# Performance work log

Hardware: AMD Instinct MI355X
Metric: run time of the kernel (lower is better)

## Reference

```python
import jax, jax.numpy as jnp
import numpy as np

B, M, K = 32, 64, 36
DS, DX, DQ, H = 512, 128, 512, 256


def setup_inputs() -> dict:
    key = jax.random.key(0)
    ks = jax.random.split(key, 11)
    sc = lambda fan_in: 1.0 / np.sqrt(fan_in)
    return {
        "s2": jax.random.normal(ks[0], (B, M, DS), jnp.float32),
        "x0": jax.random.normal(ks[1], (B, K, DX), jnp.float32),
        "q": jax.random.normal(ks[2], (B, DQ), jnp.float32),
        # score MLP: Linear(DS+DX+DQ -> H), ReLU, Linear(H -> 1)
        "score_w1": jax.random.normal(ks[3], (DS + DX + DQ, H), jnp.float32) * sc(DS + DX + DQ),
        "score_b1": jax.random.normal(ks[4], (H,), jnp.float32) * 0.01,
        "score_w2": jax.random.normal(ks[5], (H, 1), jnp.float32) * sc(H),
        "score_b2": jax.random.normal(ks[6], (1,), jnp.float32) * 0.01,
        # h MLP: Linear(DS -> H), ReLU, Linear(H -> DX)
        "h_w1": jax.random.normal(ks[7], (DS, H), jnp.float32) * sc(DS),
        "h_b1": jax.random.normal(ks[8], (H,), jnp.float32) * 0.01,
        "h_w2": jax.random.normal(ks[9], (H, DX), jnp.float32) * sc(H),
        "h_b2": jax.random.normal(ks[10], (DX,), jnp.float32) * 0.01,
    }


def reference(s2, x0, q, score_w1, score_b1, score_w2, score_b2, h_w1, h_b1, h_w2, h_b2):
    ds = s2.shape[-1]
    dx = x0.shape[-1]
    # First score Linear over concat [s_exp, x_exp, q_exp] decomposes into
    # block matmuls (same math as Linear on the concat, no 4D concat tensor).
    w_s = score_w1[:ds]            # (DS, H)
    w_x = score_w1[ds:ds + dx]     # (DX, H)
    w_q = score_w1[ds + dx:]       # (DQ, H)
    pre_s = jnp.einsum('bmd,dh->bmh', s2, w_s)   # (b, m, H)
    pre_x = jnp.einsum('bkd,dh->bkh', x0, w_x)   # (b, k, H)
    pre_q = q @ w_q                              # (b, H)
    hidden = jax.nn.relu(pre_s[:, :, None, :] + pre_x[:, None, :, :]
                         + pre_q[:, None, None, :] + score_b1)  # (b, m, k, H)
    logits = jnp.einsum('bmkh,h->bmk', hidden, score_w2[:, 0]) + score_b2[0]
    att = jax.nn.softmax(logits, axis=1)         # softmax over m
    h_s = jax.nn.relu(s2 @ h_w1 + h_b1) @ h_w2 + h_b2  # (b, m, DX)
    agg = jnp.einsum('bmk,bmf->bkf', att, h_s)   # (b, k, DX)
    return jnp.concatenate([x0, agg], axis=-1)   # (b, k, 2*DX)
```

## Files before the change

kernel.cpp:

```cpp
#include <hip/hip_runtime.h>

#define B_  32
#define M_  64
#define K_  36
#define DS_ 512
#define DX_ 128
#define DQ_ 512
#define H_  256

#define TMA  16
#define DCH  128
#define KB   9

__global__ __launch_bounds__(256) void kernA(
    const float* __restrict__ s2,
    const float* __restrict__ score_w1,
    const float* __restrict__ h_w1,
    const float* __restrict__ q,
    const float* __restrict__ score_b1,
    const float* __restrict__ x0,
    float* __restrict__ pre_s,
    float* __restrict__ ph1,
    float* __restrict__ cvec)
{
    const int t   = threadIdx.x;
    const int bid = blockIdx.x;

    if (bid >= 1024) {
        const int cb = bid - 1024;
        const int b  = cb >> 2;
        const int kq = cb & 3;
        const float* qp = q + (size_t)b * DQ_;
        const float* wq = score_w1 + (size_t)(DS_ + DX_) * H_ + t;
        float a0 = score_b1[t], a1 = 0.f, a2 = 0.f, a3 = 0.f;
        for (int d = 0; d < DQ_; d += 4) {
            const float4 q4 = *(const float4*)(qp + d);
            a0 = fmaf(q4.x, wq[(size_t)(d + 0) * H_], a0);
            a1 = fmaf(q4.y, wq[(size_t)(d + 1) * H_], a1);
            a2 = fmaf(q4.z, wq[(size_t)(d + 2) * H_], a2);
            a3 = fmaf(q4.w, wq[(size_t)(d + 3) * H_], a3);
        }
        const float qacc = (a0 + a1) + (a2 + a3);

        float acc[KB];
        #pragma unroll
        for (int kk = 0; kk < KB; ++kk) acc[kk] = qacc;

        const float* xsrc = x0 + ((size_t)b * K_ + kq * KB) * DX_;
        const float* wx   = score_w1 + (size_t)DS_ * H_ + t;
        for (int d = 0; d < DX_; d += 4) {
            const float w0 = wx[(size_t)(d + 0) * H_];
            const float w1 = wx[(size_t)(d + 1) * H_];
            const float w2v = wx[(size_t)(d + 2) * H_];
            const float w3 = wx[(size_t)(d + 3) * H_];
            #pragma unroll
            for (int kk = 0; kk < KB; ++kk) {
                const float4 x4 = *(const float4*)(xsrc + (size_t)kk * DX_ + d);
                acc[kk] = fmaf(x4.x, w0, acc[kk]);
                acc[kk] = fmaf(x4.y, w1, acc[kk]);
                acc[kk] = fmaf(x4.z, w2v, acc[kk]);
                acc[kk] = fmaf(x4.w, w3, acc[kk]);
            }
        }
        #pragma unroll
        for (int kk = 0; kk < KB; ++kk)
            cvec[((size_t)b * K_ + kq * KB + kk) * H_ + t] = acc[kk];
        return;
    }

    const int tile = bid >> 3;
    const int mat  = bid & 1;
    const int dq   = (bid >> 1) & 3;

    const float* w  = (mat ? h_w1 : score_w1) + (size_t)(dq * DCH) * H_ + t;
    const float* sp = s2 + (size_t)tile * TMA * DS_ + dq * DCH;

    float acc[TMA];
    #pragma unroll
    for (int i = 0; i < TMA; ++i) acc[i] = 0.f;

    for (int d = 0; d < DCH; d += 4) {
        const float w0 = w[(size_t)(d + 0) * H_];
        const float w1 = w[(size_t)(d + 1) * H_];
        const float w2v = w[(size_t)(d + 2) * H_];
        const float w3 = w[(size_t)(d + 3) * H_];
        #pragma unroll
        for (int i = 0; i < TMA; ++i) {
            const float4 s4 = *(const float4*)(sp + (size_t)i * DS_ + d);
            acc[i] = fmaf(s4.x, w0, acc[i]);
            acc[i] = fmaf(s4.y, w1, acc[i]);
            acc[i] = fmaf(s4.z, w2v, acc[i]);
            acc[i] = fmaf(s4.w, w3, acc[i]);
        }
    }

    float* dst = (mat ? ph1 : pre_s) + (size_t)tile * TMA * H_ + t;
    #pragma unroll
    for (int i = 0; i < TMA; ++i)
        atomicAdd(dst + (size_t)i * H_, acc[i]);
}

__global__ __launch_bounds__(256) void kernH(
    const float* __restrict__ ph1,
    const float* __restrict__ h_b1,
    const float* __restrict__ h_w2,
    float* __restrict__ h_s)
{
    __shared__ float sh[4][DCH];
    const int t    = threadIdx.x;
    const int tile = blockIdx.x >> 1;
    const int hh   = blockIdx.x & 1;
    const int r0   = tile * 4;

    if (t < 128) {
        const int row = t >> 5, j4 = (t & 31) * 4;
        const float4 p = *(const float4*)(ph1 + (size_t)(r0 + row) * H_ + hh * DCH + j4);
        const float4 b = *(const float4*)(h_b1 + hh * DCH + j4);
        float4 r;
        r.x = fmaxf(p.x + b.x, 0.f);
        r.y = fmaxf(p.y + b.y, 0.f);
        r.z = fmaxf(p.z + b.z, 0.f);
        r.w = fmaxf(p.w + b.w, 0.f);
        *(float4*)&sh[row][j4] = r;
    }
    __syncthreads();

    const int f  = t & 127;
    const int rp = t >> 7;
    const float* wp = h_w2 + (size_t)(hh * DCH) * DX_ + f;
    float acc0 = 0.f, acc1 = 0.f;
    #pragma unroll 4
    for (int h = 0; h < DCH; ++h) {
        const float wv = wp[(size_t)h * DX_];
        acc0 = fmaf(sh[rp * 2 + 0][h], wv, acc0);
        acc1 = fmaf(sh[rp * 2 + 1][h], wv, acc1);
    }
    atomicAdd(h_s + (size_t)(r0 + rp * 2 + 0) * DX_ + f, acc0);
    atomicAdd(h_s + (size_t)(r0 + rp * 2 + 1) * DX_ + f, acc1);
}

__global__ __launch_bounds__(256) void kernC(
    const float* __restrict__ pre_s,
    const float* __restrict__ h_s,
    const float* __restrict__ cvec,
    const float* __restrict__ score_w2,
    const float* __restrict__ h_b2,
    const float* __restrict__ x0,
    float* __restrict__ out)
{
    __shared__ float  red[M_][65];
    __shared__ float  att[M_];
    __shared__ float4 part[8][32];

    const int t    = threadIdx.x;
    const int bk   = blockIdx.x;
    const int b    = bk / K_;
    const int wave = t >> 6, lane = t & 63;

    const float4 cf = *(const float4*)(cvec + (size_t)bk * H_ + 4 * lane);
    const float4 wf = *(const float4*)(score_w2 + 4 * lane);

    const float* ps = pre_s + (size_t)b * M_ * H_;
    #pragma unroll 4
    for (int mi = 0; mi < M_ / 4; ++mi) {
        const int m = wave * (M_ / 4) + mi;
        const float4 p = *(const float4*)(ps + (size_t)m * H_ + 4 * lane);
        red[m][lane] = fmaxf(p.x + cf.x, 0.f) * wf.x
                     + fmaxf(p.y + cf.y, 0.f) * wf.y
                     + fmaxf(p.z + cf.z, 0.f) * wf.z
                     + fmaxf(p.w + cf.w, 0.f) * wf.w;
    }
    __syncthreads();

    if (wave == 0) {
        float a0 = 0.f, a1 = 0.f, a2 = 0.f, a3 = 0.f;
        #pragma unroll 4
        for (int l = 0; l < 64; l += 4) {
            a0 += red[lane][l + 0];
            a1 += red[lane][l + 1];
            a2 += red[lane][l + 2];
            a3 += red[lane][l + 3];
        }
        const float L = (a0 + a1) + (a2 + a3);
        float mx = L;
        #pragma unroll
        for (int off = 32; off > 0; off >>= 1)
            mx = fmaxf(mx, __shfl_xor(mx, off, 64));
        const float e = expf(L - mx);
        float s = e;
        #pragma unroll
        for (int off = 32; off > 0; off >>= 1)
            s += __shfl_xor(s, off, 64);
        att[lane] = e / s;
    }
    __syncthreads();

    {
        const int g = t >> 5, l32 = t & 31;
        const float* hp = h_s + ((size_t)b * M_ + g * 8) * DX_ + 4 * l32;
        float4 acc = make_float4(0.f, 0.f, 0.f, 0.f);
        #pragma unroll
        for (int j = 0; j < 8; ++j) {
            const float a = att[g * 8 + j];
            const float4 hv = *(const float4*)(hp + (size_t)j * DX_);
            acc.x = fmaf(a, hv.x, acc.x);
            acc.y = fmaf(a, hv.y, acc.y);
            acc.z = fmaf(a, hv.z, acc.z);
            acc.w = fmaf(a, hv.w, acc.w);
        }
        part[g][l32] = acc;
    }
    __syncthreads();

    const float4* x04 = (const float4*)(x0 + (size_t)bk * DX_);
    float4* o4 = (float4*)(out + (size_t)bk * 2 * DX_);
    if (t < 32) {
        float4 s = part[0][t];
        #pragma unroll
        for (int j = 1; j < 8; ++j) {
            const float4 p = part[j][t];
            s.x += p.x; s.y += p.y; s.z += p.z; s.w += p.w;
        }
        const float4 b2 = *(const float4*)(h_b2 + 4 * t);
        s.x += b2.x; s.y += b2.y; s.z += b2.z; s.w += b2.w;
        o4[32 + t] = s;
    } else if (t < 64) {
        o4[t - 32] = x04[t - 32];
    }
}

extern "C" void kernel_launch(void* const* d_in, const int* in_sizes, int n_in,
                              void* d_out, int out_size, void* d_ws, size_t ws_size,
                              hipStream_t stream) {
    (void)in_sizes; (void)n_in; (void)out_size; (void)ws_size;
    const float* s2       = (const float*)d_in[0];
    const float* x0       = (const float*)d_in[1];
    const float* q        = (const float*)d_in[2];
    const float* score_w1 = (const float*)d_in[3];
    const float* score_b1 = (const float*)d_in[4];
    const float* score_w2 = (const float*)d_in[5];
    const float* h_w1     = (const float*)d_in[7];
    const float* h_b1     = (const float*)d_in[8];
    const float* h_w2     = (const float*)d_in[9];
    const float* h_b2     = (const float*)d_in[10];
    float* out = (float*)d_out;

    float* ws    = (float*)d_ws;
    float* pre_s = ws;
    float* ph1   = pre_s + (size_t)B_ * M_ * H_;
    float* h_s   = ph1   + (size_t)B_ * M_ * H_;
    float* cvec  = h_s   + (size_t)B_ * M_ * DX_;

    hipMemsetAsync(d_ws, 0,
                   (size_t)B_ * M_ * (H_ + H_ + DX_) * sizeof(float), stream);

    kernA<<<1152, 256, 0, stream>>>(s2, score_w1, h_w1, q, score_b1, x0,
                                    pre_s, ph1, cvec);
    kernH<<<1024, 256, 0, stream>>>(ph1, h_b1, h_w2, h_s);
    kernC<<<B_ * K_, 256, 0, stream>>>(pre_s, h_s, cvec, score_w2, h_b2,
                                       x0, out);
}
```

Baseline: 139.5 us.

## Fold second h-MLP layer after attention, drop kernH, retile s2 GEMM

```diff
diff --git a/kernel.cpp b/kernel.cpp
--- a/kernel.cpp
+++ b/kernel.cpp
@@ -11,6 +11,12 @@
 #define TMA  16
 #define DCH  128
 #define KB   9
+
+#define FMA4(acc, sv, wv)              \
+    acc.x = fmaf(sv, wv.x, acc.x);     \
+    acc.y = fmaf(sv, wv.y, acc.y);     \
+    acc.z = fmaf(sv, wv.z, acc.z);     \
+    acc.w = fmaf(sv, wv.w, acc.w);
 
 __global__ __launch_bounds__(256) void kernA(
     const float* __restrict__ s2,
@@ -26,8 +32,8 @@
     const int t   = threadIdx.x;
     const int bid = blockIdx.x;
 
-    if (bid >= 1024) {
-        const int cb = bid - 1024;
+    if (bid < 128) {
+        const int cb = bid;
         const int b  = cb >> 2;
         const int kq = cb & 3;
         const float* qp = q + (size_t)b * DQ_;
@@ -68,89 +74,68 @@
         return;
     }
 
-    const int tile = bid >> 3;
-    const int mat  = bid & 1;
-    const int dq   = (bid >> 1) & 3;
-
-    const float* w  = (mat ? h_w1 : score_w1) + (size_t)(dq * DCH) * H_ + t;
-    const float* sp = s2 + (size_t)tile * TMA * DS_ + dq * DCH;
-
-    float acc[TMA];
+    const int g    = bid - 128;
+    const int tile = g & 127;
+    const int mc   = g >> 7;
+    const int mat  = mc & 1;
+    const int dq   = mc >> 1;
+    const int lane = t & 63;
+    const int wid  = __builtin_amdgcn_readfirstlane(t >> 6);
+
+    const float4* wq = (const float4*)((mat ? h_w1 : score_w1)
+                                       + (size_t)(dq * DCH) * H_ + 4 * lane);
+    const float* srow = s2 + (size_t)(tile * TMA + wid * 4) * DS_ + dq * DCH;
+
+    float4 acc0 = {0,0,0,0}, acc1 = {0,0,0,0}, acc2 = {0,0,0,0}, acc3 = {0,0,0,0};
+    float4 c0 = wq[0], c1 = wq[64], c2 = wq[128], c3 = wq[192];
+
+    for (int d4 = 0; d4 < DCH; d4 += 4) {
+        const int dn = (d4 + 4 < DCH) ? d4 + 4 : d4;
+        const float4 n0 = wq[(size_t)(dn + 0) * 64];
+        const float4 n1 = wq[(size_t)(dn + 1) * 64];
+        const float4 n2 = wq[(size_t)(dn + 2) * 64];
+        const float4 n3 = wq[(size_t)(dn + 3) * 64];
+
+        const float4 s0 = *(const float4*)(srow + 0 * DS_ + d4);
+        const float4 s1 = *(const float4*)(srow + 1 * DS_ + d4);
+        const float4 s2v = *(const float4*)(srow + 2 * DS_ + d4);
+        const float4 s3 = *(const float4*)(srow + 3 * DS_ + d4);
+
+        FMA4(acc0, s0.x, c0)  FMA4(acc0, s0.y, c1)  FMA4(acc0, s0.z, c2)  FMA4(acc0, s0.w, c3)
+        FMA4(acc1, s1.x, c0)  FMA4(acc1, s1.y, c1)  FMA4(acc1, s1.z, c2)  FMA4(acc1, s1.w, c3)
+        FMA4(acc2, s2v.x, c0) FMA4(acc2, s2v.y, c1) FMA4(acc2, s2v.z, c2) FMA4(acc2, s2v.w, c3)
+        FMA4(acc3, s3.x, c0)  FMA4(acc3, s3.y, c1)  FMA4(acc3, s3.z, c2)  FMA4(acc3, s3.w, c3)
+
+        c0 = n0; c1 = n1; c2 = n2; c3 = n3;
+    }
+
+    float* dst = (mat ? ph1 : pre_s)
+               + (size_t)(tile * TMA + wid * 4) * H_ + 4 * lane;
     #pragma unroll
-    for (int i = 0; i < TMA; ++i) acc[i] = 0.f;
-
-    for (int d = 0; d < DCH; d += 4) {
-        const float w0 = w[(size_t)(d + 0) * H_];
-        const float w1 = w[(size_t)(d + 1) * H_];
-        const float w2v = w[(size_t)(d + 2) * H_];
-        const float w3 = w[(size_t)(d + 3) * H_];
-        #pragma unroll
-        for (int i = 0; i < TMA; ++i) {
-            const float4 s4 = *(const float4*)(sp + (size_t)i * DS_ + d);
-            acc[i] = fmaf(s4.x, w0, acc[i]);
-            acc[i] = fmaf(s4.y, w1, acc[i]);
-            acc[i] = fmaf(s4.z, w2v, acc[i]);
-            acc[i] = fmaf(s4.w, w3, acc[i]);
-        }
-    }
-
-    float* dst = (mat ? ph1 : pre_s) + (size_t)tile * TMA * H_ + t;
-    #pragma unroll
-    for (int i = 0; i < TMA; ++i)
-        atomicAdd(dst + (size_t)i * H_, acc[i]);
+    for (int r = 0; r < 4; ++r) {
+        const float4 a = (r == 0) ? acc0 : (r == 1) ? acc1 : (r == 2) ? acc2 : acc3;
+        atomicAdd(dst + (size_t)r * H_ + 0, a.x);
+        atomicAdd(dst + (size_t)r * H_ + 1, a.y);
+        atomicAdd(dst + (size_t)r * H_ + 2, a.z);
+        atomicAdd(dst + (size_t)r * H_ + 3, a.w);
+    }
 }
 
-__global__ __launch_bounds__(256) void kernH(
+__global__ __launch_bounds__(256) void kernC(
+    const float* __restrict__ pre_s,
     const float* __restrict__ ph1,
+    const float* __restrict__ cvec,
+    const float* __restrict__ score_w2,
     const float* __restrict__ h_b1,
     const float* __restrict__ h_w2,
-    float* __restrict__ h_s)
-{
-    __shared__ float sh[4][DCH];
-    const int t    = threadIdx.x;
-    const int tile = blockIdx.x >> 1;
-    const int hh   = blockIdx.x & 1;
-    const int r0   = tile * 4;
-
-    if (t < 128) {
-        const int row = t >> 5, j4 = (t & 31) * 4;
-        const float4 p = *(const float4*)(ph1 + (size_t)(r0 + row) * H_ + hh * DCH + j4);
-        const float4 b = *(const float4*)(h_b1 + hh * DCH + j4);
-        float4 r;
-        r.x = fmaxf(p.x + b.x, 0.f);
-        r.y = fmaxf(p.y + b.y, 0.f);
-        r.z = fmaxf(p.z + b.z, 0.f);
-        r.w = fmaxf(p.w + b.w, 0.f);
-        *(float4*)&sh[row][j4] = r;
-    }
-    __syncthreads();
-
-    const int f  = t & 127;
-    const int rp = t >> 7;
-    const float* wp = h_w2 + (size_t)(hh * DCH) * DX_ + f;
-    float acc0 = 0.f, acc1 = 0.f;
-    #pragma unroll 4
-    for (int h = 0; h < DCH; ++h) {
-        const float wv = wp[(size_t)h * DX_];
-        acc0 = fmaf(sh[rp * 2 + 0][h], wv, acc0);
-        acc1 = fmaf(sh[rp * 2 + 1][h], wv, acc1);
-    }
-    atomicAdd(h_s + (size_t)(r0 + rp * 2 + 0) * DX_ + f, acc0);
-    atomicAdd(h_s + (size_t)(r0 + rp * 2 + 1) * DX_ + f, acc1);
-}
-
-__global__ __launch_bounds__(256) void kernC(
-    const float* __restrict__ pre_s,
-    const float* __restrict__ h_s,
-    const float* __restrict__ cvec,
-    const float* __restrict__ score_w2,
     const float* __restrict__ h_b2,
     const float* __restrict__ x0,
     float* __restrict__ out)
 {
-    __shared__ float  red[M_][65];
-    __shared__ float  att[M_];
-    __shared__ float4 part[8][32];
+    __shared__ float red[M_][65];
+    __shared__ float att[M_];
+    __shared__ float cw[H_];
+    __shared__ float part[DX_];
 
     const int t    = threadIdx.x;
     const int bk   = blockIdx.x;
@@ -196,36 +181,37 @@
     __syncthreads();
 
     {
-        const int g = t >> 5, l32 = t & 31;
-        const float* hp = h_s + ((size_t)b * M_ + g * 8) * DX_ + 4 * l32;
-        float4 acc = make_float4(0.f, 0.f, 0.f, 0.f);
-        #pragma unroll
-        for (int j = 0; j < 8; ++j) {
-            const float a = att[g * 8 + j];
-            const float4 hv = *(const float4*)(hp + (size_t)j * DX_);
-            acc.x = fmaf(a, hv.x, acc.x);
-            acc.y = fmaf(a, hv.y, acc.y);
-            acc.z = fmaf(a, hv.z, acc.z);
-            acc.w = fmaf(a, hv.w, acc.w);
-        }
-        part[g][l32] = acc;
-    }
-    __syncthreads();
-
-    const float4* x04 = (const float4*)(x0 + (size_t)bk * DX_);
-    float4* o4 = (float4*)(out + (size_t)bk * 2 * DX_);
-    if (t < 32) {
-        float4 s = part[0][t];
-        #pragma unroll
-        for (int j = 1; j < 8; ++j) {
-            const float4 p = part[j][t];
-            s.x += p.x; s.y += p.y; s.z += p.z; s.w += p.w;
-        }
-        const float4 b2 = *(const float4*)(h_b2 + 4 * t);
-        s.x += b2.x; s.y += b2.y; s.z += b2.z; s.w += b2.w;
-        o4[32 + t] = s;
-    } else if (t < 64) {
-        o4[t - 32] = x04[t - 32];
+        const float* hp = ph1 + (size_t)b * M_ * H_ + t;
+        const float b1v = h_b1[t];
+        float r0 = 0.f, r1 = 0.f;
+        #pragma unroll 8
+        for (int m = 0; m < M_; m += 2) {
+            r0 = fmaf(att[m],     fmaxf(hp[(size_t)m * H_] + b1v, 0.f), r0);
+            r1 = fmaf(att[m + 1], fmaxf(hp[(size_t)(m + 1) * H_] + b1v, 0.f), r1);
+        }
+        cw[t] = r0 + r1;
+    }
+    __syncthreads();
+
+    const int f  = t & 127;
+    const int hh = t >> 7;
+    const float* wp = h_w2 + (size_t)(hh * 128) * DX_ + f;
+    float a0 = 0.f, a1 = 0.f, a2 = 0.f, a3 = 0.f;
+    for (int h = 0; h < 128; h += 4) {
+        a0 = fmaf(cw[hh * 128 + h + 0], wp[(size_t)(h + 0) * DX_], a0);
+        a1 = fmaf(cw[hh * 128 + h + 1], wp[(size_t)(h + 1) * DX_], a1);
+        a2 = fmaf(cw[hh * 128 + h + 2], wp[(size_t)(h + 2) * DX_], a2);
+        a3 = fmaf(cw[hh * 128 + h + 3], wp[(size_t)(h + 3) * DX_], a3);
+    }
+    const float sum = (a0 + a1) + (a2 + a3);
+    if (hh) part[f] = sum;
+    __syncthreads();
+
+    float* o = out + (size_t)bk * (2 * DX_);
+    if (!hh) {
+        o[DX_ + f] = sum + part[f] + h_b2[f];
+    } else {
+        o[f] = x0[(size_t)bk * DX_ + f];
     }
 }
 
@@ -248,15 +234,12 @@
     float* ws    = (float*)d_ws;
     float* pre_s = ws;
     float* ph1   = pre_s + (size_t)B_ * M_ * H_;
-    float* h_s   = ph1   + (size_t)B_ * M_ * H_;
-    float* cvec  = h_s   + (size_t)B_ * M_ * DX_;
-
-    hipMemsetAsync(d_ws, 0,
-                   (size_t)B_ * M_ * (H_ + H_ + DX_) * sizeof(float), stream);
+    float* cvec  = ph1   + (size_t)B_ * M_ * H_;
+
+    hipMemsetAsync(d_ws, 0, (size_t)2 * B_ * M_ * H_ * sizeof(float), stream);
 
     kernA<<<1152, 256, 0, stream>>>(s2, score_w1, h_w1, q, score_b1, x0,
                                     pre_s, ph1, cvec);
-    kernH<<<1024, 256, 0, stream>>>(ph1, h_b1, h_w2, h_s);
-    kernC<<<B_ * K_, 256, 0, stream>>>(pre_s, h_s, cvec, score_w2, h_b2,
-                                       x0, out);
+    kernC<<<B_ * K_, 256, 0, stream>>>(pre_s, ph1, cvec, score_w2, h_b1,
+                                       h_w2, h_b2, x0, out);
 }
```

After: 156.7 us. 1.12x slower.
